# Optimization experiments

Measured on AMD Instinct MI355X. Metric: run time of the kernel, lower is better.

The kernel has to match this reference:

```python
import jax, jax.numpy as jnp
import numpy as np

T_STEPS = 128
N_RAYS = 16384
RAY_EXT = 10.0  # ray_ext_factor


def _posenc(x, n_freq=4):
    # x: (...,3) in [-1,1] -> (...,3 + 3*2*n_freq) = (...,27)
    feats = [x]
    for k in range(n_freq):
        f = (2.0 ** k) * jnp.pi
        feats.append(jnp.sin(f * x))
        feats.append(jnp.cos(f * x))
    return jnp.concatenate(feats, -1)


def _sh_deg2(d):
    # real spherical harmonics, degree 0 and 1 (4 coeffs), d unit vectors (...,3)
    x, y, z = d[..., 0], d[..., 1], d[..., 2]
    c0 = 0.28209479177387814
    c1 = 0.4886025119029199
    return jnp.stack([jnp.full_like(x, c0), c1 * y, c1 * z, c1 * x], -1)


def _forward(rays_o, rays_d, tnoise, aabb, W1, b1, W2, b2, Wc1, bc1, Wc2, bc2):
    # --- ray-AABB intersection (slab method), RayBundle.intersect_aabb ---
    inv_d = 1.0 / rays_d
    t0 = (aabb[0] - rays_o) * inv_d
    t1 = (aabb[1] - rays_o) * inv_d
    tnear = jnp.maximum(jnp.max(jnp.minimum(t0, t1), -1, keepdims=True), 0.0)  # (N,1)
    tfar = jnp.min(jnp.maximum(t0, t1), -1, keepdims=True)                      # (N,1)
    active = (tfar > tnear).astype(rays_o.dtype)  # active_mask; masking replaces compaction

    # --- StratifiedRayStepSampler: ts (T,N,1) ---
    T = tnoise.shape[0]
    base = (jnp.arange(T, dtype=rays_o.dtype)[:, None, None] + tnoise) / T
    ts = tnear[None] + (tfar - tnear)[None] * base
    xyz = rays_o[None] + ts * rays_d[None]  # (T,N,3)

    # --- vol.sample(xyz, ynm, return_color=True): density + color MLP ---
    xn = 2.0 * (xyz - aabb[0]) / (aabb[1] - aabb[0]) - 1.0
    enc = _posenc(xn)                             # (T,N,27)
    h = jax.nn.relu(enc @ W1 + b1)                # (T,N,64)
    dh = h @ W2 + b2                              # (T,N,16)
    sigma = jnp.exp(dh[..., :1])                  # (T,N,1) density
    feat = dh[..., 1:]                            # (T,N,15)
    dnorm = jnp.linalg.norm(rays_d, axis=-1, keepdims=True)  # (N,1)
    ynm = _sh_deg2(rays_d / dnorm)                # encode_raydir -> (N,4)
    ynm = jnp.broadcast_to(ynm[None], (T,) + ynm.shape)      # expand to (T,N,4)
    hc = jax.nn.relu(jnp.concatenate([feat, ynm], -1) @ Wc1 + bc1)
    rgb = jax.nn.sigmoid(hc @ Wc2 + bc2)          # (T,N,3)

    # --- integrate_timesteps: transmittance-weighted compositing ---
    tfinal = tfar * RAY_EXT
    delta = jnp.concatenate([ts[1:] - ts[:-1], tfinal[None] - ts[-1:]], 0)  # (T,N,1)
    sd = sigma * delta * dnorm[None]
    alpha = 1.0 - jnp.exp(-sd)
    trans = jnp.exp(-(jnp.cumsum(sd, 0) - sd))    # exclusive cumsum transmittance
    w = trans * alpha * active[None]              # (T,N,1); inactive rays -> zero maps

    color = jnp.sum(w * rgb, 0)                   # color_map  (N,3)
    alpha_map = jnp.sum(w, 0)                     # alpha_map  (N,1)
    return jnp.concatenate([color, alpha_map], -1)  # rgba (N,4)


def setup_inputs() -> dict:
    key = jax.random.key(0)
    ks = jax.random.split(key, 8)
    # origins on a sphere of radius 2.5 around the unit aabb, aimed at points inside it
    o = jax.random.normal(ks[0], (N_RAYS, 3), jnp.float32)
    o = 2.5 * o / jnp.linalg.norm(o, axis=-1, keepdims=True)
    tgt = jax.random.uniform(ks[1], (N_RAYS, 3), jnp.float32, -0.5, 0.5)
    d = tgt - o
    d = d / jnp.linalg.norm(d, axis=-1, keepdims=True)
    aabb = jnp.array([[-1.0, -1.0, -1.0], [1.0, 1.0, 1.0]], jnp.float32)
    tnoise = jax.random.uniform(ks[2], (T_STEPS, N_RAYS, 1), jnp.float32)
    s1, s2, s3, s4 = 27 ** -0.5, 64 ** -0.5, 19 ** -0.5, 64 ** -0.5
    return {
        'rays_o': o, 'rays_d': d, 'tnoise': tnoise, 'aabb': aabb,
        'W1': jax.random.normal(ks[3], (27, 64), jnp.float32) * s1,
        'b1': jnp.zeros((64,), jnp.float32),
        'W2': jax.random.normal(ks[4], (64, 16), jnp.float32) * (0.1 * s2),
        'b2': jnp.zeros((16,), jnp.float32),
        'Wc1': jax.random.normal(ks[5], (19, 64), jnp.float32) * s3,
        'bc1': jnp.zeros((64,), jnp.float32),
        'Wc2': jax.random.normal(ks[6], (64, 3), jnp.float32) * s4,
        'bc2': jnp.zeros((3,), jnp.float32),
    }


def reference(rays_o, rays_d, tnoise, aabb, W1, b1, W2, b2, Wc1, bc1, Wc2, bc2):
    return _forward(rays_o, rays_d, tnoise, aabb, W1, b1, W2, b2, Wc1, bc1, Wc2, bc2)
```

## Files before the change

kernel.cpp:

```cpp
#include <hip/hip_runtime.h>
#include <stdint.h>

#define N_RAYS  16384
#define T_STEPS 128
#define RPW   16
#define WAVES 8
#define TSEG  16

typedef _Float16 half8  __attribute__((ext_vector_type(8)));
typedef _Float16 half4  __attribute__((ext_vector_type(4)));
typedef __fp16   fp16x2 __attribute__((ext_vector_type(2)));
typedef float    float4_ __attribute__((ext_vector_type(4)));

#define LOG2E 1.4426950408889634f
#define LOG2_LOG2E 0.5287663729448977f

#define H8_W1    0
#define H_W2K16  2048
#define H_WC2K16 3072
#define H_WC1K16 4096
#define F32_CV   3072
#define F32_BC2  3392
#define F32_S0   3408

__device__ __forceinline__ uint32_t pk(float a, float b) {
    fp16x2 h = __builtin_amdgcn_cvt_pkrtz(a, b);
    return __builtin_bit_cast(uint32_t, h);
}
__device__ __forceinline__ uint32_t pkr(float a, float b) {
    fp16x2 h = __builtin_amdgcn_cvt_pkrtz(a, b);
    fp16x2 z = {(__fp16)0.f, (__fp16)0.f};
    fp16x2 m = __builtin_elementwise_max(h, z);
    return __builtin_bit_cast(uint32_t, m);
}

__global__ void prep_weights(const float* __restrict__ W1, const float* __restrict__ b1,
                             const float* __restrict__ W2, const float* __restrict__ b2,
                             const float* __restrict__ Wc1, const float* __restrict__ bc1,
                             const float* __restrict__ Wc2, const float* __restrict__ bc2,
                             void* __restrict__ ws) {
    _Float16* wh = (_Float16*)ws;
    float*    wf = (float*)ws;
    int frag = blockIdx.x;
    int lane = threadIdx.x;
    int mm = lane & 15, q = lane >> 4;
    if (frag < 4) {
        int tau = frag;
        int n = tau * 16 + mm;
        for (int j = 0; j < 8; ++j) {
            float w;
            if (j < 6)      w = W1[(3 + 6 * q + j) * 64 + n];
            else if (j == 6) w = (q == 0) ? W1[0 * 64 + n] : (q == 1) ? W1[2 * 64 + n] : 0.f;
            else             w = (q == 0) ? W1[1 * 64 + n] : (q == 1) ? b1[n] : 0.f;
            wh[(H8_W1 + tau * 64 + lane) * 8 + j] = (_Float16)w;
        }
    } else if (frag < 8) {
        int tau = frag - 4;
        for (int j = 0; j < 4; ++j) {
            int k = tau * 16 + 4 * q + j;
            float v = W2[k * 16 + mm];
            if (mm == 0) v *= LOG2E;
            wh[H_W2K16 + (tau * 64 + lane) * 4 + j] = (_Float16)v;
        }
    } else if (frag < 12) {
        int tau = frag - 8;
        int n2 = tau * 16 + mm;
        for (int j = 0; j < 4; ++j) {
            int k = 4 * q + j;
            float w = (k == 0) ? 0.f : Wc1[(k - 1) * 64 + n2];
            wh[H_WC1K16 + (tau * 64 + lane) * 4 + j] = (_Float16)w;
        }
    } else if (frag < 16) {
        int tau = frag - 12;
        for (int j = 0; j < 4; ++j) {
            int k = tau * 16 + 4 * q + j;
            wh[H_WC2K16 + (tau * 64 + lane) * 4 + j] =
                (_Float16)((mm < 12) ? Wc2[k * 3 + (mm >> 2)] * LOG2E : 0.f);
        }
    } else {
        int n = lane;
        wf[F32_CV + 0 * 64 + n] = Wc1[15 * 64 + n];
        wf[F32_CV + 1 * 64 + n] = Wc1[16 * 64 + n];
        wf[F32_CV + 2 * 64 + n] = Wc1[17 * 64 + n];
        wf[F32_CV + 3 * 64 + n] = Wc1[18 * 64 + n];
        float cc = bc1[n];
        for (int c = 0; c < 15; ++c) cc += b2[1 + c] * Wc1[c * 64 + n];
        wf[F32_CV + 4 * 64 + n] = cc;
        if (lane < 16) wf[F32_BC2 + lane] = (lane < 12) ? bc2[lane >> 2] * LOG2E : 0.f;
        if (lane == 0) wf[F32_S0] = b2[0] * LOG2E + LOG2_LOG2E;
    }
}

__global__ __launch_bounds__(512, 4)
void render_kernel(const float* __restrict__ rays_o, const float* __restrict__ rays_d,
                   const float* __restrict__ tnoise, const float* __restrict__ aabb,
                   const void* __restrict__ ws, float* __restrict__ out) {
    __shared__ float sComb[WAVES][RPW][4];

    const int tid  = threadIdx.x;
    const int wv   = tid >> 6;
    const int lane = tid & 63;
    const int m    = lane & 15;
    const int q    = lane >> 4;
    const int r    = blockIdx.x * RPW + m;

    const half8* wsv  = (const half8*)ws;
    const half4* w2v  = (const half4*)((const _Float16*)ws + H_W2K16);
    const half4* wc2v = (const half4*)((const _Float16*)ws + H_WC2K16);
    const half4* wc1v = (const half4*)((const _Float16*)ws + H_WC1K16);
    const float* wsf  = (const float*)ws;
    half8 fW1[4];
    half4 fW2[4], fWc1[4], fWc2[4];
    #pragma unroll
    for (int i = 0; i < 4; ++i) fW1[i]  = wsv[H8_W1 + i * 64 + lane];
    #pragma unroll
    for (int i = 0; i < 4; ++i) fW2[i]  = w2v[i * 64 + lane];
    #pragma unroll
    for (int i = 0; i < 4; ++i) fWc1[i] = wc1v[i * 64 + lane];
    #pragma unroll
    for (int i = 0; i < 4; ++i) fWc2[i] = wc2v[i * 64 + lane];
    const float4_ binit = ((const float4_*)(wsf + F32_BC2))[q];

    float o0 = rays_o[r * 3 + 0], o1 = rays_o[r * 3 + 1], o2 = rays_o[r * 3 + 2];
    float d0 = rays_d[r * 3 + 0], d1 = rays_d[r * 3 + 1], d2 = rays_d[r * 3 + 2];
    float a00 = aabb[0], a01 = aabb[1], a02 = aabb[2];
    float a10 = aabb[3], a11 = aabb[4], a12 = aabb[5];

    float i0 = 1.0f / d0, i1 = 1.0f / d1, i2 = 1.0f / d2;
    float u0 = (a00 - o0) * i0, v0 = (a10 - o0) * i0;
    float u1 = (a01 - o1) * i1, v1 = (a11 - o1) * i1;
    float u2 = (a02 - o2) * i2, v2 = (a12 - o2) * i2;
    float tnear = fmaxf(fmaxf(fmaxf(fminf(u0, v0), fminf(u1, v1)), fminf(u2, v2)), 0.0f);
    float tfar  = fminf(fminf(fmaxf(u0, v0), fmaxf(u1, v1)), fmaxf(u2, v2));
    bool active = (tfar > tnear);
    float dt = tfar - tnear;
    float dt128 = dt * (1.0f / 128.0f);

    float dn  = sqrtf(d0 * d0 + d1 * d1 + d2 * d2);
    float idn = 1.0f / dn;
    const float s0r = wsf[F32_S0] + __builtin_amdgcn_logf(dn);
    const float c0sh = 0.28209479177387814f;
    const float c1sh = 0.4886025119029199f;
    float y1 = c1sh * d1 * idn, y2 = c1sh * d2 * idn, y3 = c1sh * d0 * idn;

    float4_ cv[4];
    #pragma unroll
    for (int tau = 0; tau < 4; ++tau) {
        #pragma unroll
        for (int reg = 0; reg < 4; ++reg) {
            int n = tau * 16 + 4 * q + reg;
            float c = wsf[F32_CV + 4 * 64 + n];
            c = fmaf(c0sh, wsf[F32_CV + 0 * 64 + n], c);
            c = fmaf(y1,   wsf[F32_CV + 1 * 64 + n], c);
            c = fmaf(y2,   wsf[F32_CV + 2 * 64 + n], c);
            c = fmaf(y3,   wsf[F32_CV + 3 * 64 + n], c);
            cv[tau][reg] = c;
        }
    }

    float qs = 0.5f * (float)(1 << q);
    float sc0 = 2.0f / (a10 - a00), of0 = -a00 * sc0 - 1.0f;
    float sc1 = 2.0f / (a11 - a01), of1 = -a01 * sc1 - 1.0f;
    float sc2 = 2.0f / (a12 - a02), of2 = -a02 * sc2 - 1.0f;
    float kq0 = d0 * (sc0 * qs), bq0 = fmaf(o0, sc0 * qs, of0 * qs);
    float kq1 = d1 * (sc1 * qs), bq1 = fmaf(o1, sc1 * qs, of1 * qs);
    float kq2 = d2 * (sc2 * qs), bq2 = fmaf(o2, sc2 * qs, of2 * qs);

    const float4_ z4 = {0.f, 0.f, 0.f, 0.f};
    const bool q0 = (q == 0), q1 = (q == 1);
    const float c6 = q0 ? 2.0f : (q1 ? 1.0f : 0.0f);
    const float c7a = q0 ? 2.0f : 0.0f;
    const float c7b = q1 ? 1.0f : 0.0f;

    float trans = 1.0f;
    float cacc = 0.0f;

    const int tbase = wv * TSEG;
    float nA = tnoise[(tbase + 0) * N_RAYS + r];
    float nB = tnoise[(tbase + 1) * N_RAYS + r];

    #pragma unroll 2
    for (int tt = 0; tt < TSEG; tt += 2) {
        const int t0 = tbase + tt, t1 = t0 + 1;
        int ic = t0 + 2; if (ic > T_STEPS - 1) ic = T_STEPS - 1;
        int id = t0 + 3; if (id > T_STEPS - 1) id = T_STEPS - 1;
        float nC = tnoise[ic * N_RAYS + r];
        float nD = tnoise[id * N_RAYS + r];
        float ts0 = fmaf((float)t0 + nA, dt128, tnear);
        float ts1 = fmaf((float)t1 + nB, dt128, tnear);
        float ts2 = fmaf((float)(t0 + 2) + nC, dt128, tnear);
        float tsP[2] = {ts0, ts1};
        float deltaP[2];
        deltaP[0] = ts1 - ts0;
        deltaP[1] = (t1 < T_STEPS - 1) ? (ts2 - ts1) : fmaf(tfar, 10.0f, -ts1);
        nA = nC; nB = nD;

        float dhx[2];
        float4_ rgbP[2];

        #pragma unroll
        for (int p = 0; p < 2; ++p) {
            float xr0 = fmaf(tsP[p], kq0, bq0);
            float xr1 = fmaf(tsP[p], kq1, bq1);
            float xr2 = fmaf(tsP[p], kq2, bq2);
            float s0 = __builtin_amdgcn_sinf(xr0);
            float s1 = __builtin_amdgcn_sinf(xr1);
            float s2 = __builtin_amdgcn_sinf(xr2);
            float cA = __builtin_amdgcn_cosf(xr0);
            float cB = __builtin_amdgcn_cosf(xr1);
            float cC = __builtin_amdgcn_cosf(xr2);
            float e6 = c6 * (q0 ? xr0 : xr2);
            float e7 = fmaf(xr1, c7a, c7b);
            union { uint32_t u[4]; half8 h; } xf_;
            xf_.u[0] = pk(s0, s1); xf_.u[1] = pk(s2, cA);
            xf_.u[2] = pk(cB, cC); xf_.u[3] = pk(e6, e7);
            half8 xf = xf_.h;

            float4_ h0 = __builtin_amdgcn_mfma_f32_16x16x32_f16(fW1[0], xf, z4, 0, 0, 0);
            float4_ h1 = __builtin_amdgcn_mfma_f32_16x16x32_f16(fW1[1], xf, z4, 0, 0, 0);
            float4_ h2 = __builtin_amdgcn_mfma_f32_16x16x32_f16(fW1[2], xf, z4, 0, 0, 0);
            float4_ h3 = __builtin_amdgcn_mfma_f32_16x16x32_f16(fW1[3], xf, z4, 0, 0, 0);

            union { uint32_t u[2]; half4 h; } hb0_, hb1_, hb2_, hb3_;
            hb0_.u[0] = pkr(h0.x, h0.y); hb0_.u[1] = pkr(h0.z, h0.w);
            hb1_.u[0] = pkr(h1.x, h1.y); hb1_.u[1] = pkr(h1.z, h1.w);
            hb2_.u[0] = pkr(h2.x, h2.y); hb2_.u[1] = pkr(h2.z, h2.w);
            hb3_.u[0] = pkr(h3.x, h3.y); hb3_.u[1] = pkr(h3.z, h3.w);

            float4_ dh = __builtin_amdgcn_mfma_f32_16x16x16f16(fW2[0], hb0_.h, z4, 0, 0, 0);
            dh = __builtin_amdgcn_mfma_f32_16x16x16f16(fW2[1], hb1_.h, dh, 0, 0, 0);
            dh = __builtin_amdgcn_mfma_f32_16x16x16f16(fW2[2], hb2_.h, dh, 0, 0, 0);
            dh = __builtin_amdgcn_mfma_f32_16x16x16f16(fW2[3], hb3_.h, dh, 0, 0, 0);

            dhx[p] = __shfl(dh.x, m, 64);

            union { uint32_t u[2]; half4 h; } fb_;
            fb_.u[0] = pk(dh.x, dh.y); fb_.u[1] = pk(dh.z, dh.w);
            half4 fb = fb_.h;

            float4_ t0v = __builtin_amdgcn_mfma_f32_16x16x16f16(fWc1[0], fb, cv[0], 0, 0, 0);
            float4_ t1v = __builtin_amdgcn_mfma_f32_16x16x16f16(fWc1[1], fb, cv[1], 0, 0, 0);
            float4_ t2v = __builtin_amdgcn_mfma_f32_16x16x16f16(fWc1[2], fb, cv[2], 0, 0, 0);
            float4_ t3v = __builtin_amdgcn_mfma_f32_16x16x16f16(fWc1[3], fb, cv[3], 0, 0, 0);

            union { uint32_t u[2]; half4 h; } cb0_, cb1_, cb2_, cb3_;
            cb0_.u[0] = pkr(t0v.x, t0v.y); cb0_.u[1] = pkr(t0v.z, t0v.w);
            cb1_.u[0] = pkr(t1v.x, t1v.y); cb1_.u[1] = pkr(t1v.z, t1v.w);
            cb2_.u[0] = pkr(t2v.x, t2v.y); cb2_.u[1] = pkr(t2v.z, t2v.w);
            cb3_.u[0] = pkr(t3v.x, t3v.y); cb3_.u[1] = pkr(t3v.z, t3v.w);

            float4_ rr4 = __builtin_amdgcn_mfma_f32_16x16x16f16(fWc2[0], cb0_.h, binit, 0, 0, 0);
            rr4 = __builtin_amdgcn_mfma_f32_16x16x16f16(fWc2[1], cb1_.h, rr4, 0, 0, 0);
            rr4 = __builtin_amdgcn_mfma_f32_16x16x16f16(fWc2[2], cb2_.h, rr4, 0, 0, 0);
            rr4 = __builtin_amdgcn_mfma_f32_16x16x16f16(fWc2[3], cb3_.h, rr4, 0, 0, 0);
            rgbP[p] = rr4;
        }

        #pragma unroll
        for (int p = 0; p < 2; ++p) {
            float sg = __builtin_amdgcn_exp2f(dhx[p] + s0r);
            float sd = sg * deltaP[p];
            float e  = __builtin_amdgcn_exp2f(-sd);
            float s  = __builtin_amdgcn_rcpf(1.0f + __builtin_amdgcn_exp2f(-rgbP[p].x));
            float tn = trans * e;
            cacc = fmaf(trans - tn, s, cacc);
            trans = tn;
        }
    }

    if (q == 3) sComb[wv][m][0] = trans;
    else        sComb[wv][m][1 + q] = cacc;
    __syncthreads();

    if (tid < RPW) {
        float P = 1.0f, C0 = 0.0f, C1 = 0.0f, C2 = 0.0f;
        #pragma unroll
        for (int s = 0; s < WAVES; ++s) {
            C0 = fmaf(P, sComb[s][tid][1], C0);
            C1 = fmaf(P, sComb[s][tid][2], C1);
            C2 = fmaf(P, sComb[s][tid][3], C2);
            P *= sComb[s][tid][0];
        }
        float act = active ? 1.0f : 0.0f;
        const int rg = blockIdx.x * RPW + tid;
        out[rg * 4 + 0] = C0 * act;
        out[rg * 4 + 1] = C1 * act;
        out[rg * 4 + 2] = C2 * act;
        out[rg * 4 + 3] = (1.0f - P) * act;
    }
}

extern "C" void kernel_launch(void* const* d_in, const int* in_sizes, int n_in,
                              void* d_out, int out_size, void* d_ws, size_t ws_size,
                              hipStream_t stream) {
    const float* rays_o = (const float*)d_in[0];
    const float* rays_d = (const float*)d_in[1];
    const float* tnoise = (const float*)d_in[2];
    const float* aabb   = (const float*)d_in[3];
    const float* W1  = (const float*)d_in[4];
    const float* b1  = (const float*)d_in[5];
    const float* W2  = (const float*)d_in[6];
    const float* b2  = (const float*)d_in[7];
    const float* Wc1 = (const float*)d_in[8];
    const float* bc1 = (const float*)d_in[9];
    const float* Wc2 = (const float*)d_in[10];
    const float* bc2 = (const float*)d_in[11];

    prep_weights<<<dim3(17), dim3(64), 0, stream>>>(W1, b1, W2, b2, Wc1, bc1, Wc2, bc2, d_ws);

    dim3 grid(N_RAYS / RPW);
    dim3 block(WAVES * 64);
    render_kernel<<<grid, block, 0, stream>>>(rays_o, rays_d, tnoise, aabb, d_ws,
                                              (float*)d_out);
}
```

Baseline: 118.2 us.

## Fold weight preparation into render kernel and drop separate prep launch

Removes the prep_weights kernel and has every render thread load and pack its fp32 MLP weight fragments into fp16 registers directly from the input tensors. The b2 bias is now fed as the initial accumulator of the W2 MFMA instead of being folded into precomputed constants. This saves a kernel launch and a dependency on the workspace, at the cost of redundant scattered weight loads and conversions in each of the 1024 blocks. The time loop's unroll factor also drops from 2 to 1.

```diff
diff --git a/kernel.cpp b/kernel.cpp
--- a/kernel.cpp
+++ b/kernel.cpp
@@ -14,14 +14,6 @@
 
 #define LOG2E 1.4426950408889634f
 #define LOG2_LOG2E 0.5287663729448977f
-
-#define H8_W1    0
-#define H_W2K16  2048
-#define H_WC2K16 3072
-#define H_WC1K16 4096
-#define F32_CV   3072
-#define F32_BC2  3392
-#define F32_S0   3408
 
 __device__ __forceinline__ uint32_t pk(float a, float b) {
     fp16x2 h = __builtin_amdgcn_cvt_pkrtz(a, b);
@@ -34,67 +26,14 @@
     return __builtin_bit_cast(uint32_t, m);
 }
 
-__global__ void prep_weights(const float* __restrict__ W1, const float* __restrict__ b1,
-                             const float* __restrict__ W2, const float* __restrict__ b2,
-                             const float* __restrict__ Wc1, const float* __restrict__ bc1,
-                             const float* __restrict__ Wc2, const float* __restrict__ bc2,
-                             void* __restrict__ ws) {
-    _Float16* wh = (_Float16*)ws;
-    float*    wf = (float*)ws;
-    int frag = blockIdx.x;
-    int lane = threadIdx.x;
-    int mm = lane & 15, q = lane >> 4;
-    if (frag < 4) {
-        int tau = frag;
-        int n = tau * 16 + mm;
-        for (int j = 0; j < 8; ++j) {
-            float w;
-            if (j < 6)      w = W1[(3 + 6 * q + j) * 64 + n];
-            else if (j == 6) w = (q == 0) ? W1[0 * 64 + n] : (q == 1) ? W1[2 * 64 + n] : 0.f;
-            else             w = (q == 0) ? W1[1 * 64 + n] : (q == 1) ? b1[n] : 0.f;
-            wh[(H8_W1 + tau * 64 + lane) * 8 + j] = (_Float16)w;
-        }
-    } else if (frag < 8) {
-        int tau = frag - 4;
-        for (int j = 0; j < 4; ++j) {
-            int k = tau * 16 + 4 * q + j;
-            float v = W2[k * 16 + mm];
-            if (mm == 0) v *= LOG2E;
-            wh[H_W2K16 + (tau * 64 + lane) * 4 + j] = (_Float16)v;
-        }
-    } else if (frag < 12) {
-        int tau = frag - 8;
-        int n2 = tau * 16 + mm;
-        for (int j = 0; j < 4; ++j) {
-            int k = 4 * q + j;
-            float w = (k == 0) ? 0.f : Wc1[(k - 1) * 64 + n2];
-            wh[H_WC1K16 + (tau * 64 + lane) * 4 + j] = (_Float16)w;
-        }
-    } else if (frag < 16) {
-        int tau = frag - 12;
-        for (int j = 0; j < 4; ++j) {
-            int k = tau * 16 + 4 * q + j;
-            wh[H_WC2K16 + (tau * 64 + lane) * 4 + j] =
-                (_Float16)((mm < 12) ? Wc2[k * 3 + (mm >> 2)] * LOG2E : 0.f);
-        }
-    } else {
-        int n = lane;
-        wf[F32_CV + 0 * 64 + n] = Wc1[15 * 64 + n];
-        wf[F32_CV + 1 * 64 + n] = Wc1[16 * 64 + n];
-        wf[F32_CV + 2 * 64 + n] = Wc1[17 * 64 + n];
-        wf[F32_CV + 3 * 64 + n] = Wc1[18 * 64 + n];
-        float cc = bc1[n];
-        for (int c = 0; c < 15; ++c) cc += b2[1 + c] * Wc1[c * 64 + n];
-        wf[F32_CV + 4 * 64 + n] = cc;
-        if (lane < 16) wf[F32_BC2 + lane] = (lane < 12) ? bc2[lane >> 2] * LOG2E : 0.f;
-        if (lane == 0) wf[F32_S0] = b2[0] * LOG2E + LOG2_LOG2E;
-    }
-}
-
 __global__ __launch_bounds__(512, 4)
 void render_kernel(const float* __restrict__ rays_o, const float* __restrict__ rays_d,
                    const float* __restrict__ tnoise, const float* __restrict__ aabb,
-                   const void* __restrict__ ws, float* __restrict__ out) {
+                   const float* __restrict__ W1, const float* __restrict__ b1,
+                   const float* __restrict__ W2, const float* __restrict__ b2,
+                   const float* __restrict__ Wc1, const float* __restrict__ bc1,
+                   const float* __restrict__ Wc2, const float* __restrict__ bc2,
+                   float* __restrict__ out) {
     __shared__ float sComb[WAVES][RPW][4];
 
     const int tid  = threadIdx.x;
@@ -104,22 +43,72 @@
     const int q    = lane >> 4;
     const int r    = blockIdx.x * RPW + m;
 
-    const half8* wsv  = (const half8*)ws;
-    const half4* w2v  = (const half4*)((const _Float16*)ws + H_W2K16);
-    const half4* wc2v = (const half4*)((const _Float16*)ws + H_WC2K16);
-    const half4* wc1v = (const half4*)((const _Float16*)ws + H_WC1K16);
-    const float* wsf  = (const float*)ws;
+    const bool q0 = (q == 0), q1 = (q == 1);
+
     half8 fW1[4];
-    half4 fW2[4], fWc1[4], fWc2[4];
-    #pragma unroll
-    for (int i = 0; i < 4; ++i) fW1[i]  = wsv[H8_W1 + i * 64 + lane];
-    #pragma unroll
-    for (int i = 0; i < 4; ++i) fW2[i]  = w2v[i * 64 + lane];
-    #pragma unroll
-    for (int i = 0; i < 4; ++i) fWc1[i] = wc1v[i * 64 + lane];
-    #pragma unroll
-    for (int i = 0; i < 4; ++i) fWc2[i] = wc2v[i * 64 + lane];
-    const float4_ binit = ((const float4_*)(wsf + F32_BC2))[q];
+    #pragma unroll
+    for (int tau = 0; tau < 4; ++tau) {
+        int n = tau * 16 + m;
+        float v0 = W1[(3 + 6 * q + 0) * 64 + n];
+        float v1 = W1[(3 + 6 * q + 1) * 64 + n];
+        float v2 = W1[(3 + 6 * q + 2) * 64 + n];
+        float v3 = W1[(3 + 6 * q + 3) * 64 + n];
+        float v4 = W1[(3 + 6 * q + 4) * 64 + n];
+        float v5 = W1[(3 + 6 * q + 5) * 64 + n];
+        float v6 = q0 ? W1[0 * 64 + n] : (q1 ? W1[2 * 64 + n] : 0.f);
+        float v7 = q0 ? W1[1 * 64 + n] : (q1 ? b1[n] : 0.f);
+        union { uint32_t u[4]; half8 h; } t;
+        t.u[0] = pk(v0, v1); t.u[1] = pk(v2, v3);
+        t.u[2] = pk(v4, v5); t.u[3] = pk(v6, v7);
+        fW1[tau] = t.h;
+    }
+    half4 fW2[4];
+    #pragma unroll
+    for (int tau = 0; tau < 4; ++tau) {
+        float v[4];
+        #pragma unroll
+        for (int j = 0; j < 4; ++j) {
+            int k = tau * 16 + 4 * q + j;
+            v[j] = W2[k * 16 + m];
+        }
+        if (m == 0) { v[0] *= LOG2E; v[1] *= LOG2E; v[2] *= LOG2E; v[3] *= LOG2E; }
+        union { uint32_t u[2]; half4 h; } t;
+        t.u[0] = pk(v[0], v[1]); t.u[1] = pk(v[2], v[3]);
+        fW2[tau] = t.h;
+    }
+    half4 fWc1[4];
+    #pragma unroll
+    for (int tau = 0; tau < 4; ++tau) {
+        int n2 = tau * 16 + m;
+        float v[4];
+        #pragma unroll
+        for (int j = 0; j < 4; ++j) {
+            int k = 4 * q + j;
+            v[j] = (k == 0) ? 0.f : Wc1[(k - 1) * 64 + n2];
+        }
+        union { uint32_t u[2]; half4 h; } t;
+        t.u[0] = pk(v[0], v[1]); t.u[1] = pk(v[2], v[3]);
+        fWc1[tau] = t.h;
+    }
+    half4 fWc2[4];
+    #pragma unroll
+    for (int tau = 0; tau < 4; ++tau) {
+        float v[4];
+        #pragma unroll
+        for (int j = 0; j < 4; ++j) {
+            int k = tau * 16 + 4 * q + j;
+            v[j] = (m < 12) ? Wc2[k * 3 + (m >> 2)] * LOG2E : 0.f;
+        }
+        union { uint32_t u[2]; half4 h; } t;
+        t.u[0] = pk(v[0], v[1]); t.u[1] = pk(v[2], v[3]);
+        fWc2[tau] = t.h;
+    }
+    float4_ b2v;
+    #pragma unroll
+    for (int j = 0; j < 4; ++j) b2v[j] = b2[4 * q + j];
+    if (q0) b2v[0] *= LOG2E;
+    float bb = (q < 3) ? bc2[q] * LOG2E : 0.0f;
+    const float4_ binit = {bb, bb, bb, bb};
 
     float o0 = rays_o[r * 3 + 0], o1 = rays_o[r * 3 + 1], o2 = rays_o[r * 3 + 2];
     float d0 = rays_d[r * 3 + 0], d1 = rays_d[r * 3 + 1], d2 = rays_d[r * 3 + 2];
@@ -138,7 +127,7 @@
 
     float dn  = sqrtf(d0 * d0 + d1 * d1 + d2 * d2);
     float idn = 1.0f / dn;
-    const float s0r = wsf[F32_S0] + __builtin_amdgcn_logf(dn);
+    const float s0r = LOG2_LOG2E + __builtin_amdgcn_logf(dn);
     const float c0sh = 0.28209479177387814f;
     const float c1sh = 0.4886025119029199f;
     float y1 = c1sh * d1 * idn, y2 = c1sh * d2 * idn, y3 = c1sh * d0 * idn;
@@ -149,11 +138,11 @@
         #pragma unroll
         for (int reg = 0; reg < 4; ++reg) {
             int n = tau * 16 + 4 * q + reg;
-            float c = wsf[F32_CV + 4 * 64 + n];
-            c = fmaf(c0sh, wsf[F32_CV + 0 * 64 + n], c);
-            c = fmaf(y1,   wsf[F32_CV + 1 * 64 + n], c);
-            c = fmaf(y2,   wsf[F32_CV + 2 * 64 + n], c);
-            c = fmaf(y3,   wsf[F32_CV + 3 * 64 + n], c);
+            float c = bc1[n];
+            c = fmaf(c0sh, Wc1[15 * 64 + n], c);
+            c = fmaf(y1,   Wc1[16 * 64 + n], c);
+            c = fmaf(y2,   Wc1[17 * 64 + n], c);
+            c = fmaf(y3,   Wc1[18 * 64 + n], c);
             cv[tau][reg] = c;
         }
     }
@@ -167,7 +156,6 @@
     float kq2 = d2 * (sc2 * qs), bq2 = fmaf(o2, sc2 * qs, of2 * qs);
 
     const float4_ z4 = {0.f, 0.f, 0.f, 0.f};
-    const bool q0 = (q == 0), q1 = (q == 1);
     const float c6 = q0 ? 2.0f : (q1 ? 1.0f : 0.0f);
     const float c7a = q0 ? 2.0f : 0.0f;
     const float c7b = q1 ? 1.0f : 0.0f;
@@ -179,7 +167,7 @@
     float nA = tnoise[(tbase + 0) * N_RAYS + r];
     float nB = tnoise[(tbase + 1) * N_RAYS + r];
 
-    #pragma unroll 2
+    #pragma unroll 1
     for (int tt = 0; tt < TSEG; tt += 2) {
         const int t0 = tbase + tt, t1 = t0 + 1;
         int ic = t0 + 2; if (ic > T_STEPS - 1) ic = T_STEPS - 1;
@@ -227,7 +215,7 @@
             hb2_.u[0] = pkr(h2.x, h2.y); hb2_.u[1] = pkr(h2.z, h2.w);
             hb3_.u[0] = pkr(h3.x, h3.y); hb3_.u[1] = pkr(h3.z, h3.w);
 
-            float4_ dh = __builtin_amdgcn_mfma_f32_16x16x16f16(fW2[0], hb0_.h, z4, 0, 0, 0);
+            float4_ dh = __builtin_amdgcn_mfma_f32_16x16x16f16(fW2[0], hb0_.h, b2v, 0, 0, 0);
             dh = __builtin_amdgcn_mfma_f32_16x16x16f16(fW2[1], hb1_.h, dh, 0, 0, 0);
             dh = __builtin_amdgcn_mfma_f32_16x16x16f16(fW2[2], hb2_.h, dh, 0, 0, 0);
             dh = __builtin_amdgcn_mfma_f32_16x16x16f16(fW2[3], hb3_.h, dh, 0, 0, 0);
@@ -306,10 +294,9 @@
     const float* Wc2 = (const float*)d_in[10];
     const float* bc2 = (const float*)d_in[11];
 
-    prep_weights<<<dim3(17), dim3(64), 0, stream>>>(W1, b1, W2, b2, Wc1, bc1, Wc2, bc2, d_ws);
-
     dim3 grid(N_RAYS / RPW);
     dim3 block(WAVES * 64);
-    render_kernel<<<grid, block, 0, stream>>>(rays_o, rays_d, tnoise, aabb, d_ws,
+    render_kernel<<<grid, block, 0, stream>>>(rays_o, rays_d, tnoise, aabb,
+                                              W1, b1, W2, b2, Wc1, bc1, Wc2, bc2,
                                               (float*)d_out);
 }
```

Result: slower. 125.5 us (+6.2%).
